# Kernel optimization log

Hardware: AMD Instinct MI355X
Metric: run time of the kernel (lower is better)

## Reference

```python
import jax, jax.numpy as jnp
import numpy as np

# nuScenes-style config: 6 cams, 4 FPN levels of a 256x704 image
SPATIAL = np.array([[64, 176], [32, 88], [16, 44], [8, 22]], dtype=np.int32)  # (H, W) per level
NUM_CAMS = 6
EMBED = 256      # embed dims C
GROUPS = 8       # attention groups, C % GROUPS == 0
BS = 2
ANCHORS = 900    # queries
PTS = 13         # key points per anchor


def setup_inputs() -> dict:
    key = jax.random.key(0)
    k1, k2, k3 = jax.random.split(key, 3)
    hw = SPATIAL.prod(axis=1)                                   # per-level H*W
    starts = np.concatenate([[0], np.cumsum(hw)[:-1]]).astype(np.int32)
    num_value = NUM_CAMS * int(hw.sum())                        # 6 * 14960 = 89760
    value = jax.random.normal(k1, (BS, num_value, EMBED), jnp.float32)
    input_spatial_shapes = jnp.asarray(np.tile(SPATIAL[None], (NUM_CAMS, 1, 1)))   # [cams, lvls, 2]
    input_level_start_index = jnp.asarray(np.tile(starts[None], (NUM_CAMS, 1)))    # [cams, lvls]
    sampling_locations = jax.random.uniform(k2, (BS, ANCHORS, PTS, NUM_CAMS, 2), jnp.float32)
    attention_weights = jax.random.uniform(k3, (BS, ANCHORS, PTS, NUM_CAMS, SPATIAL.shape[0], GROUPS), jnp.float32)
    return {
        "value": value,
        "input_spatial_shapes": input_spatial_shapes,
        "input_level_start_index": input_level_start_index,
        "sampling_locations": sampling_locations,
        "attention_weights": attention_weights,
    }


def _dfa(value, shapes, starts, loc, weights):
    """Multi-scale multi-camera deformable aggregation (Sparse4D kernel math)."""
    bs, num_value, c = value.shape
    num_cams, num_levels = shapes.shape[:2]
    _, A, P = loc.shape[:3]
    groups = weights.shape[-1]
    gdim = c // groups
    per_cam = num_value // num_cams
    value_c = value.reshape(bs, num_cams, per_cam, c)           # cam-major layout
    b_idx = jnp.arange(bs)[:, None, None, None]
    cam_idx = jnp.arange(num_cams)[None, None, None, :]
    loc_w = loc[..., 0]                                          # [bs, A, P, cams]
    loc_h = loc[..., 1]
    out = jnp.zeros((bs, A, groups, gdim), value.dtype)
    for lvl in range(num_levels):                                # static small loop over levels
        H = int(shapes[0, lvl, 0]); W = int(shapes[0, lvl, 1]); s = int(starts[0, lvl])
        featf = value_c[:, :, s:s + H * W, :]                    # [bs, cams, H*W, c]
        h = loc_h * H - 0.5
        w = loc_w * W - 0.5
        h0 = jnp.floor(h); w0 = jnp.floor(w)
        dh = h - h0; dw = w - w0
        h0i = h0.astype(jnp.int32); w0i = w0.astype(jnp.int32)

        def corner(hi, wi, bw):
            valid = (hi >= 0) & (hi < H) & (wi >= 0) & (wi < W)  # zero padding outside
            idx = jnp.clip(hi, 0, H - 1) * W + jnp.clip(wi, 0, W - 1)
            v = featf[b_idx, cam_idx, idx]                       # gather -> [bs, A, P, cams, c]
            return v * (bw * valid)[..., None]

        samp = (corner(h0i,     w0i,     (1 - dh) * (1 - dw))
              + corner(h0i,     w0i + 1, (1 - dh) * dw)
              + corner(h0i + 1, w0i,     dh * (1 - dw))
              + corner(h0i + 1, w0i + 1, dh * dw))               # bilinear sample [bs, A, P, cams, c]
        samp = samp.reshape(bs, A, P, num_cams, groups, gdim)
        out = out + jnp.einsum("bapcgd,bapcg->bagd", samp, weights[..., lvl, :])
    return out.reshape(bs, A, c)


def reference(value, input_spatial_shapes, input_level_start_index, sampling_locations, attention_weights):
    shapes = np.asarray(input_spatial_shapes)
    starts = np.asarray(input_level_start_index)
    return _dfa(value, shapes, starts, sampling_locations, attention_weights)
```

## Files before the change

### kernel.cpp

```cpp
#include <hip/hip_runtime.h>
#include <hip/hip_fp16.h>

constexpr int NCAMS   = 6;
constexpr int EMB     = 256;
constexpr int NGROUPS = 8;
constexpr int NLVL    = 4;
constexpr int NPTS    = 13;
constexpr int NPAIR   = NPTS * NCAMS;
constexpr int NWAVES  = 8;


__global__ __launch_bounds__(256)
void cvt_kernel(const float4* __restrict__ in, ushort4* __restrict__ out, int n4)
{
    for (int i = blockIdx.x * blockDim.x + threadIdx.x; i < n4;
         i += gridDim.x * blockDim.x) {
        const float4 v = in[i];
        ushort4 h;
        h.x = __half_as_ushort(__float2half_rn(v.x));
        h.y = __half_as_ushort(__float2half_rn(v.y));
        h.z = __half_as_ushort(__float2half_rn(v.z));
        h.w = __half_as_ushort(__float2half_rn(v.w));
        out[i] = h;
    }
}

__device__ __forceinline__ void issue_pair_h(
    int pair,
    const __half* __restrict__ hval,
    const float* __restrict__ locp,
    const float* __restrict__ awp_g,
    int b, int per_cam, int half_id, int side,
    const int H_[NLVL], const int W_[NLVL], const int S_[NLVL],
    uint4 d[8], float wg[8])
{
    const int c = pair % NCAMS;
    const float lw = locp[pair * 2 + 0];
    const float lh = locp[pair * 2 + 1];
    const __half* vb = hval + ((long)(b * NCAMS + c) * per_cam) * EMB + half_id * 8;
    const float* awpc = awp_g + pair * (NLVL * NGROUPS);

    #pragma unroll
    for (int lvl = 0; lvl < NLVL; ++lvl) {
        const int H = H_[lvl], W = W_[lvl], S = S_[lvl];
        const float hf = lh * (float)H - 0.5f;
        const float wf = lw * (float)W - 0.5f;
        const float h0f = floorf(hf), w0f = floorf(wf);
        const float dh = hf - h0f, dw = wf - w0f;
        const int h0 = (int)h0f, w0 = (int)w0f;
        const int h1 = h0 + 1;
        const int wS = w0 + side;

        const float aw = awpc[lvl * NGROUPS];
        const float cw = side ? dw : (1.f - dw);

        const bool vw  = (unsigned)wS < (unsigned)W;
        const bool vh0 = (unsigned)h0 < (unsigned)H;
        const bool vh1 = (unsigned)h1 < (unsigned)H;
        float wt = (1.f - dh) * cw * aw;
        float wb = dh         * cw * aw;
        wt = (vh0 && vw) ? wt : 0.f;
        wb = (vh1 && vw) ? wb : 0.f;

        const int wc  = min(max(wS, 0), W - 1);
        const int h0c = min(max(h0, 0), H - 1);
        const int h1c = min(max(h1, 0), H - 1);

        d[lvl * 2 + 0] = *(const uint4*)(vb + (long)(S + h0c * W + wc) * EMB);
        d[lvl * 2 + 1] = *(const uint4*)(vb + (long)(S + h1c * W + wc) * EMB);
        wg[lvl * 2 + 0] = wt;
        wg[lvl * 2 + 1] = wb;
    }
}

__device__ __forceinline__ void consume_pair_h(const uint4 d[8], const float wg[8],
                                               float acc[8])
{
    #pragma unroll
    for (int k = 0; k < 8; ++k) {
        const float w = wg[k];
        const uint4 v = d[k];
        const __half2* h2 = reinterpret_cast<const __half2*>(&v);
        #pragma unroll
        for (int q = 0; q < 4; ++q) {
            const float2 f = __half22float2(h2[q]);
            acc[2 * q + 0] = fmaf(f.x, w, acc[2 * q + 0]);
            acc[2 * q + 1] = fmaf(f.y, w, acc[2 * q + 1]);
        }
    }
}

__global__ __launch_bounds__(512)
void dfa_kernel_h(const __half* __restrict__ hval,
                  const int*   __restrict__ shapes,
                  const int*   __restrict__ starts,
                  const float* __restrict__ loc,
                  const float* __restrict__ attw,
                  float*       __restrict__ out,
                  int A, int per_cam)
{
    const int tid  = threadIdx.x;
    const int wv   = tid >> 6;
    const int lane = tid & 63;
    const int b = blockIdx.x / A;
    const int a = blockIdx.x - b * A;

    __shared__ int   sH[NLVL], sW[NLVL], sS[NLVL];
    __shared__ float red[NWAVES][EMB];
    if (tid < NLVL) {
        sH[tid] = shapes[tid * 2 + 0];
        sW[tid] = shapes[tid * 2 + 1];
        sS[tid] = starts[tid];
    }
    __syncthreads();

    int H_[NLVL], W_[NLVL], S_[NLVL];
    #pragma unroll
    for (int l = 0; l < NLVL; ++l) { H_[l] = sH[l]; W_[l] = sW[l]; S_[l] = sS[l]; }

    const int half_id = lane & 31;
    const int side    = lane >> 5;
    const int g       = half_id >> 2;

    const long ba = (long)b * A + a;
    const float* locp = loc  + ba * (NPTS * NCAMS * 2);
    const float* awp  = attw + ba * (NPTS * NCAMS * NLVL * NGROUPS) + g;

    float acc[8];
    #pragma unroll
    for (int j = 0; j < 8; ++j) acc[j] = 0.f;
    uint4 dA[8], dB[8];
    float wA[8], wB[8];

    int j = wv;
    issue_pair_h(j, hval, locp, awp, b, per_cam, half_id, side, H_, W_, S_, dA, wA);
    j += NWAVES;
    while (j + NWAVES < NPAIR) {
        issue_pair_h(j, hval, locp, awp, b, per_cam, half_id, side, H_, W_, S_, dB, wB);
        consume_pair_h(dA, wA, acc);
        issue_pair_h(j + NWAVES, hval, locp, awp, b, per_cam, half_id, side, H_, W_, S_, dA, wA);
        consume_pair_h(dB, wB, acc);
        j += 2 * NWAVES;
    }
    if (j < NPAIR) {
        issue_pair_h(j, hval, locp, awp, b, per_cam, half_id, side, H_, W_, S_, dB, wB);
        consume_pair_h(dA, wA, acc);
        consume_pair_h(dB, wB, acc);
    } else {
        consume_pair_h(dA, wA, acc);
    }

    #pragma unroll
    for (int k = 0; k < 8; ++k) acc[k] += __shfl_down(acc[k], 32);

    if (lane < 32) {
        float* r = &red[wv][half_id * 8];
        *(float4*)(r + 0) = make_float4(acc[0], acc[1], acc[2], acc[3]);
        *(float4*)(r + 4) = make_float4(acc[4], acc[5], acc[6], acc[7]);
    }
    __syncthreads();

    float s0 = 0.f;
    if (tid < 256) {
        s0 = red[0][tid] + red[1][tid] + red[2][tid] + red[3][tid];
    } else {
        const int t = tid - 256;
        red[4][t] = red[4][t] + red[5][t] + red[6][t] + red[7][t];
    }
    __syncthreads();
    if (tid < 256) {
        out[ba * EMB + tid] = s0 + red[4][tid];
    }
}

__device__ __forceinline__ void issue_pair_f(
    int pair,
    const float* __restrict__ value,
    const float* __restrict__ locp,
    const float* __restrict__ awp_g,
    int b, int per_cam, int lane,
    const int H_[NLVL], const int W_[NLVL], const int S_[NLVL],
    float4 d[16], float wg[16])
{
    const int p = pair / NCAMS;
    const int c = pair - p * NCAMS;
    const float lw = locp[pair * 2 + 0];
    const float lh = locp[pair * 2 + 1];
    const float* vb = value + ((long)(b * NCAMS + c) * per_cam) * EMB + lane * 4;
    const float* awpc = awp_g + pair * (NLVL * NGROUPS);

    #pragma unroll
    for (int lvl = 0; lvl < NLVL; ++lvl) {
        const int H = H_[lvl], W = W_[lvl], S = S_[lvl];
        const float hf = lh * (float)H - 0.5f;
        const float wf = lw * (float)W - 0.5f;
        const float h0f = floorf(hf), w0f = floorf(wf);
        const float dh = hf - h0f, dw = wf - w0f;
        const int h0 = (int)h0f, w0 = (int)w0f;
        const int h1 = h0 + 1,  w1 = w0 + 1;
        const float aw = awpc[lvl * NGROUPS];
        const float w00 = (1.f - dh) * (1.f - dw) * aw;
        const float w01 = (1.f - dh) * dw         * aw;
        const float w10 = dh         * (1.f - dw) * aw;
        const float w11 = dh         * dw         * aw;
        const bool vh0 = (unsigned)h0 < (unsigned)H;
        const bool vh1 = (unsigned)h1 < (unsigned)H;
        const bool vw0 = (unsigned)w0 < (unsigned)W;
        const bool vw1 = (unsigned)w1 < (unsigned)W;
        wg[lvl * 4 + 0] = (vh0 && vw0) ? w00 : 0.f;
        wg[lvl * 4 + 1] = (vh0 && vw1) ? w01 : 0.f;
        wg[lvl * 4 + 2] = (vh1 && vw0) ? w10 : 0.f;
        wg[lvl * 4 + 3] = (vh1 && vw1) ? w11 : 0.f;
        const int h0c = min(max(h0, 0), H - 1);
        const int h1c = min(max(h1, 0), H - 1);
        const int w0c = min(max(w0, 0), W - 1);
        const int w1c = min(max(w1, 0), W - 1);
        const float* r0 = vb + (long)(S + h0c * W) * EMB;
        const float* r1 = vb + (long)(S + h1c * W) * EMB;
        d[lvl * 4 + 0] = *(const float4*)(r0 + (long)w0c * EMB);
        d[lvl * 4 + 1] = *(const float4*)(r0 + (long)w1c * EMB);
        d[lvl * 4 + 2] = *(const float4*)(r1 + (long)w0c * EMB);
        d[lvl * 4 + 3] = *(const float4*)(r1 + (long)w1c * EMB);
    }
}

__device__ __forceinline__ void consume_pair_f(const float4 d[16], const float wg[16],
                                               float4& acc)
{
    #pragma unroll
    for (int k = 0; k < 16; ++k) {
        acc.x = fmaf(d[k].x, wg[k], acc.x);
        acc.y = fmaf(d[k].y, wg[k], acc.y);
        acc.z = fmaf(d[k].z, wg[k], acc.z);
        acc.w = fmaf(d[k].w, wg[k], acc.w);
    }
}

__global__ __launch_bounds__(512)
void dfa_kernel_f(const float* __restrict__ value,
                  const int*   __restrict__ shapes,
                  const int*   __restrict__ starts,
                  const float* __restrict__ loc,
                  const float* __restrict__ attw,
                  float*       __restrict__ out,
                  int A, int per_cam)
{
    const int tid  = threadIdx.x;
    const int wv   = tid >> 6;
    const int lane = tid & 63;
    const int b = blockIdx.x / A;
    const int a = blockIdx.x - b * A;

    __shared__ int   sH[NLVL], sW[NLVL], sS[NLVL];
    __shared__ float red[NWAVES][EMB];
    if (tid < NLVL) {
        sH[tid] = shapes[tid * 2 + 0];
        sW[tid] = shapes[tid * 2 + 1];
        sS[tid] = starts[tid];
    }
    __syncthreads();

    int H_[NLVL], W_[NLVL], S_[NLVL];
    #pragma unroll
    for (int l = 0; l < NLVL; ++l) { H_[l] = sH[l]; W_[l] = sW[l]; S_[l] = sS[l]; }

    const int g = lane >> 3;
    const long ba = (long)b * A + a;
    const float* locp = loc  + ba * (NPTS * NCAMS * 2);
    const float* awp  = attw + ba * (NPTS * NCAMS * NLVL * NGROUPS) + g;

    float4 acc = make_float4(0.f, 0.f, 0.f, 0.f);
    float4 dA[16], dB[16];
    float  wA[16], wB[16];

    int j = wv;
    issue_pair_f(j, value, locp, awp, b, per_cam, lane, H_, W_, S_, dA, wA);
    j += NWAVES;
    while (j + NWAVES < NPAIR) {
        issue_pair_f(j, value, locp, awp, b, per_cam, lane, H_, W_, S_, dB, wB);
        consume_pair_f(dA, wA, acc);
        issue_pair_f(j + NWAVES, value, locp, awp, b, per_cam, lane, H_, W_, S_, dA, wA);
        consume_pair_f(dB, wB, acc);
        j += 2 * NWAVES;
    }
    if (j < NPAIR) {
        issue_pair_f(j, value, locp, awp, b, per_cam, lane, H_, W_, S_, dB, wB);
        consume_pair_f(dA, wA, acc);
        consume_pair_f(dB, wB, acc);
    } else {
        consume_pair_f(dA, wA, acc);
    }

    *(float4*)&red[wv][lane * 4] = acc;
    __syncthreads();

    float s0 = 0.f;
    if (tid < 256) {
        s0 = red[0][tid] + red[1][tid] + red[2][tid] + red[3][tid];
    } else {
        const int t = tid - 256;
        red[4][t] = red[4][t] + red[5][t] + red[6][t] + red[7][t];
    }
    __syncthreads();
    if (tid < 256) {
        out[ba * EMB + tid] = s0 + red[4][tid];
    }
}

extern "C" void kernel_launch(void* const* d_in, const int* in_sizes, int n_in,
                              void* d_out, int out_size, void* d_ws, size_t ws_size,
                              hipStream_t stream) {
    const float* value  = (const float*)d_in[0];
    const int*   shapes = (const int*)d_in[1];
    const int*   starts = (const int*)d_in[2];
    const float* loc    = (const float*)d_in[3];
    const float* attw   = (const float*)d_in[4];
    float*       out    = (float*)d_out;

    const int B = 2;
    const int A = out_size / (EMB * B);
    const int per_cam = in_sizes[0] / (B * EMB * NCAMS);

    dim3 grid(B * A);
    dim3 block(512);

    const size_t need = (size_t)in_sizes[0] * sizeof(__half);
    if (ws_size >= need) {
        __half* hval = (__half*)d_ws;
        const int n4 = in_sizes[0] / 4;
        cvt_kernel<<<2048, 256, 0, stream>>>((const float4*)value, (ushort4*)hval, n4);
        dfa_kernel_h<<<grid, block, 0, stream>>>(hval, shapes, starts, loc, attw,
                                                 out, A, per_cam);
    } else {
        dfa_kernel_f<<<grid, block, 0, stream>>>(value, shapes, starts, loc, attw,
                                                 out, A, per_cam);
    }
}
```

Measured before the change: 395.7 us.

## Precompute sampling geometry in shared memory and accumulate in packed half2

Bilinear geometry (corner offsets and weights) is now computed once per block into shared memory, and the attention weights are staged there too, so waves no longer recompute the same per-level math redundantly. The inner accumulation switches from fp32 FMAs on converted halves to packed __hfma2 in half precision. This cuts ALU work and register pressure in the gather loop, at the cost of an extra block-wide barrier and reduced accumulation precision over up to 80 terms per lane.

```diff
diff --git a/kernel.cpp b/kernel.cpp
--- a/kernel.cpp
+++ b/kernel.cpp
@@ -8,6 +8,8 @@
 constexpr int NPTS    = 13;
 constexpr int NPAIR   = NPTS * NCAMS;
 constexpr int NWAVES  = 8;
+constexpr int NGEOM   = NPAIR * NLVL * 2;
+constexpr int NAW     = NPAIR * NLVL * NGROUPS;
 
 
 __global__ __launch_bounds__(256)
@@ -25,71 +27,6 @@
     }
 }
 
-__device__ __forceinline__ void issue_pair_h(
-    int pair,
-    const __half* __restrict__ hval,
-    const float* __restrict__ locp,
-    const float* __restrict__ awp_g,
-    int b, int per_cam, int half_id, int side,
-    const int H_[NLVL], const int W_[NLVL], const int S_[NLVL],
-    uint4 d[8], float wg[8])
-{
-    const int c = pair % NCAMS;
-    const float lw = locp[pair * 2 + 0];
-    const float lh = locp[pair * 2 + 1];
-    const __half* vb = hval + ((long)(b * NCAMS + c) * per_cam) * EMB + half_id * 8;
-    const float* awpc = awp_g + pair * (NLVL * NGROUPS);
-
-    #pragma unroll
-    for (int lvl = 0; lvl < NLVL; ++lvl) {
-        const int H = H_[lvl], W = W_[lvl], S = S_[lvl];
-        const float hf = lh * (float)H - 0.5f;
-        const float wf = lw * (float)W - 0.5f;
-        const float h0f = floorf(hf), w0f = floorf(wf);
-        const float dh = hf - h0f, dw = wf - w0f;
-        const int h0 = (int)h0f, w0 = (int)w0f;
-        const int h1 = h0 + 1;
-        const int wS = w0 + side;
-
-        const float aw = awpc[lvl * NGROUPS];
-        const float cw = side ? dw : (1.f - dw);
-
-        const bool vw  = (unsigned)wS < (unsigned)W;
-        const bool vh0 = (unsigned)h0 < (unsigned)H;
-        const bool vh1 = (unsigned)h1 < (unsigned)H;
-        float wt = (1.f - dh) * cw * aw;
-        float wb = dh         * cw * aw;
-        wt = (vh0 && vw) ? wt : 0.f;
-        wb = (vh1 && vw) ? wb : 0.f;
-
-        const int wc  = min(max(wS, 0), W - 1);
-        const int h0c = min(max(h0, 0), H - 1);
-        const int h1c = min(max(h1, 0), H - 1);
-
-        d[lvl * 2 + 0] = *(const uint4*)(vb + (long)(S + h0c * W + wc) * EMB);
-        d[lvl * 2 + 1] = *(const uint4*)(vb + (long)(S + h1c * W + wc) * EMB);
-        wg[lvl * 2 + 0] = wt;
-        wg[lvl * 2 + 1] = wb;
-    }
-}
-
-__device__ __forceinline__ void consume_pair_h(const uint4 d[8], const float wg[8],
-                                               float acc[8])
-{
-    #pragma unroll
-    for (int k = 0; k < 8; ++k) {
-        const float w = wg[k];
-        const uint4 v = d[k];
-        const __half2* h2 = reinterpret_cast<const __half2*>(&v);
-        #pragma unroll
-        for (int q = 0; q < 4; ++q) {
-            const float2 f = __half22float2(h2[q]);
-            acc[2 * q + 0] = fmaf(f.x, w, acc[2 * q + 0]);
-            acc[2 * q + 1] = fmaf(f.y, w, acc[2 * q + 1]);
-        }
-    }
-}
-
 __global__ __launch_bounds__(512)
 void dfa_kernel_h(const __half* __restrict__ hval,
                   const int*   __restrict__ shapes,
@@ -105,58 +42,125 @@
     const int b = blockIdx.x / A;
     const int a = blockIdx.x - b * A;
 
-    __shared__ int   sH[NLVL], sW[NLVL], sS[NLVL];
+    __shared__ float attw_s[NAW];
+    __shared__ int   gOffT[NGEOM];
+    __shared__ int   gOffB[NGEOM];
+    __shared__ float gWT[NGEOM];
+    __shared__ float gWB[NGEOM];
     __shared__ float red[NWAVES][EMB];
-    if (tid < NLVL) {
-        sH[tid] = shapes[tid * 2 + 0];
-        sW[tid] = shapes[tid * 2 + 1];
-        sS[tid] = starts[tid];
-    }
-    __syncthreads();
-
-    int H_[NLVL], W_[NLVL], S_[NLVL];
-    #pragma unroll
-    for (int l = 0; l < NLVL; ++l) { H_[l] = sH[l]; W_[l] = sW[l]; S_[l] = sS[l]; }
+
+    const long ba = (long)b * A + a;
+    const float* locp = loc  + ba * (NPTS * NCAMS * 2);
+    const float* awp  = attw + ba * (long)NAW;
+
+    for (int i = tid; i < NAW; i += 512) attw_s[i] = awp[i];
+
+    for (int item = tid; item < NGEOM; item += 512) {
+        const int side = item & 1;
+        const int t    = item >> 1;
+        const int lvl  = t & 3;
+        const int pair = t >> 2;
+
+        const int H = shapes[lvl * 2 + 0];
+        const int W = shapes[lvl * 2 + 1];
+        const int S = starts[lvl];
+
+        const float lw = locp[pair * 2 + 0];
+        const float lh = locp[pair * 2 + 1];
+
+        const float hf = lh * (float)H - 0.5f;
+        const float wf = lw * (float)W - 0.5f;
+        const float h0f = floorf(hf), w0f = floorf(wf);
+        const float dh = hf - h0f, dw = wf - w0f;
+        const int h0 = (int)h0f, w0 = (int)w0f;
+        const int h1 = h0 + 1;
+        const int wS = w0 + side;
+
+        const float cw = side ? dw : (1.f - dw);
+        const bool vw  = (unsigned)wS < (unsigned)W;
+        const bool vh0 = (unsigned)h0 < (unsigned)H;
+        const bool vh1 = (unsigned)h1 < (unsigned)H;
+
+        gWT[item] = (vh0 && vw) ? (1.f - dh) * cw : 0.f;
+        gWB[item] = (vh1 && vw) ? dh * cw         : 0.f;
+
+        const int wc  = min(max(wS, 0), W - 1);
+        const int h0c = min(max(h0, 0), H - 1);
+        const int h1c = min(max(h1, 0), H - 1);
+        gOffT[item] = (S + h0c * W + wc) * EMB;
+        gOffB[item] = (S + h1c * W + wc) * EMB;
+    }
+    __syncthreads();
 
     const int half_id = lane & 31;
     const int side    = lane >> 5;
     const int g       = half_id >> 2;
 
-    const long ba = (long)b * A + a;
-    const float* locp = loc  + ba * (NPTS * NCAMS * 2);
-    const float* awp  = attw + ba * (NPTS * NCAMS * NLVL * NGROUPS) + g;
-
-    float acc[8];
-    #pragma unroll
-    for (int j = 0; j < 8; ++j) acc[j] = 0.f;
+    __half2 acc2[4];
+    #pragma unroll
+    for (int q = 0; q < 4; ++q) acc2[q] = __float2half2_rn(0.f);
+
     uint4 dA[8], dB[8];
-    float wA[8], wB[8];
+    __half2 wA[8], wB[8];
+
+    auto issue = [&](int pair, uint4 d[8], __half2 wg[8]) {
+        const int c = pair % NCAMS;
+        const __half* base = hval + ((long)(b * NCAMS + c) * per_cam) * EMB
+                                  + half_id * 8;
+        const int gbase = pair * (NLVL * 2) + side;
+        const int abase = pair * (NLVL * NGROUPS) + g;
+        #pragma unroll
+        for (int lvl = 0; lvl < NLVL; ++lvl) {
+            const int idx = gbase + lvl * 2;
+            const float aw = attw_s[abase + lvl * NGROUPS];
+            wg[lvl * 2 + 0] = __float2half2_rn(gWT[idx] * aw);
+            wg[lvl * 2 + 1] = __float2half2_rn(gWB[idx] * aw);
+            d[lvl * 2 + 0] = *(const uint4*)(base + gOffT[idx]);
+            d[lvl * 2 + 1] = *(const uint4*)(base + gOffB[idx]);
+        }
+    };
+    auto consume = [&](const uint4 d[8], const __half2 wg[8]) {
+        #pragma unroll
+        for (int k = 0; k < 8; ++k) {
+            const __half2* h2 = reinterpret_cast<const __half2*>(&d[k]);
+            #pragma unroll
+            for (int q = 0; q < 4; ++q)
+                acc2[q] = __hfma2(h2[q], wg[k], acc2[q]);
+        }
+    };
 
     int j = wv;
-    issue_pair_h(j, hval, locp, awp, b, per_cam, half_id, side, H_, W_, S_, dA, wA);
+    issue(j, dA, wA);
     j += NWAVES;
     while (j + NWAVES < NPAIR) {
-        issue_pair_h(j, hval, locp, awp, b, per_cam, half_id, side, H_, W_, S_, dB, wB);
-        consume_pair_h(dA, wA, acc);
-        issue_pair_h(j + NWAVES, hval, locp, awp, b, per_cam, half_id, side, H_, W_, S_, dA, wA);
-        consume_pair_h(dB, wB, acc);
+        issue(j, dB, wB);
+        consume(dA, wA);
+        issue(j + NWAVES, dA, wA);
+        consume(dB, wB);
         j += 2 * NWAVES;
     }
     if (j < NPAIR) {
-        issue_pair_h(j, hval, locp, awp, b, per_cam, half_id, side, H_, W_, S_, dB, wB);
-        consume_pair_h(dA, wA, acc);
-        consume_pair_h(dB, wB, acc);
-    } else {
-        consume_pair_h(dA, wA, acc);
-    }
-
-    #pragma unroll
-    for (int k = 0; k < 8; ++k) acc[k] += __shfl_down(acc[k], 32);
+        issue(j, dB, wB);
+        consume(dA, wA);
+        consume(dB, wB);
+    } else {
+        consume(dA, wA);
+    }
+
+    float af[8];
+    #pragma unroll
+    for (int q = 0; q < 4; ++q) {
+        const float2 f = __half22float2(acc2[q]);
+        af[2 * q + 0] = f.x;
+        af[2 * q + 1] = f.y;
+    }
+    #pragma unroll
+    for (int k = 0; k < 8; ++k) af[k] += __shfl_down(af[k], 32);
 
     if (lane < 32) {
         float* r = &red[wv][half_id * 8];
-        *(float4*)(r + 0) = make_float4(acc[0], acc[1], acc[2], acc[3]);
-        *(float4*)(r + 4) = make_float4(acc[4], acc[5], acc[6], acc[7]);
+        *(float4*)(r + 0) = make_float4(af[0], af[1], af[2], af[3]);
+        *(float4*)(r + 4) = make_float4(af[4], af[5], af[6], af[7]);
     }
     __syncthreads();
 
```

After: 378.3 us. 4.4% less time.
